# Kernel tuning notes

Measured on AMD Instinct MI355X. Metric: run time of the kernel, lower is better.

Reference implementation:

```python
import jax, jax.numpy as jnp
import numpy as np

N, M, K = 40000, 20000, 16
IN_DIM, HID, OUT_DIM, H = 64, 128, 128, 4
DH = HID // H
SIGMA_A = 15.0
FACTOR_A = 180.0 / (SIGMA_A * np.pi)  # angle (rad) -> embedding index, GeoTransformer convention
EPS = 1e-5


def sinusoidal_embed(x, d_model):
    """GeoTransformer-style sinusoidal embedding, interleaved [sin0,cos0,sin1,cos1,...]."""
    div = jnp.exp(jnp.arange(0, d_model, 2, dtype=jnp.float32) * (-np.log(10000.0) / d_model))
    omegas = x[..., None] * div  # (..., d_model/2)
    emb = jnp.stack([jnp.sin(omegas), jnp.cos(omegas)], axis=-1)
    return emb.reshape(*x.shape, d_model)


def setup_inputs() -> dict:
    key = jax.random.key(0)
    ks = jax.random.split(key, 16)

    def lin(k, i, o):
        return jax.random.normal(k, (i, o), jnp.float32) * (1.0 / np.sqrt(i))

    return {
        "feats": jax.random.normal(ks[0], (N, IN_DIM), jnp.float32),
        "node_idx": jax.random.randint(ks[1], (M,), 0, N, dtype=jnp.int32),
        "group_idx": jax.random.randint(ks[2], (M, K), 0, N, dtype=jnp.int32),
        "ppfs": jax.random.uniform(ks[3], (M, K, 4), jnp.float32, 0.0, np.pi),
        # PPF structural embedding projection
        "W_a": lin(ks[4], HID, HID), "b_a": jnp.zeros((HID,), jnp.float32),
        # input projection
        "W_in": lin(ks[5], IN_DIM, HID), "b_in": jnp.zeros((HID,), jnp.float32),
        # attention q/k/v/p projections
        "W_q": lin(ks[6], HID, HID), "b_q": jnp.zeros((HID,), jnp.float32),
        "W_k": lin(ks[7], HID, HID), "b_k": jnp.zeros((HID,), jnp.float32),
        "W_v": lin(ks[8], HID, HID), "b_v": jnp.zeros((HID,), jnp.float32),
        "W_p": lin(ks[9], HID, HID), "b_p": jnp.zeros((HID,), jnp.float32),
        # attention output linear + layernorm
        "W_o": lin(ks[10], HID, HID), "b_o": jnp.zeros((HID,), jnp.float32),
        "ln_g": jnp.ones((HID,), jnp.float32), "ln_b": jnp.zeros((HID,), jnp.float32),
        # output projection
        "W_out": lin(ks[11], HID, OUT_DIM), "b_out": jnp.zeros((OUT_DIM,), jnp.float32),
    }


def reference(feats, node_idx, group_idx, ppfs,
              W_a, b_a, W_in, b_in, W_q, b_q, W_k, b_k, W_v, b_v, W_p, b_p,
              W_o, b_o, ln_g, ln_b, W_out, b_out):
    # --- PPF structural embedding: sinusoidal per angle, linear, max over 4 angles ---
    a_emb = sinusoidal_embed(ppfs * FACTOR_A, HID)          # (M, K, 4, HID)
    a_emb = a_emb @ W_a + b_a
    pos = jnp.max(a_emb, axis=2)                            # (M, K, HID)

    # --- input projection ---
    f = feats @ W_in + b_in                                 # (N, HID)

    # --- local RPE multi-head attention ---
    q = (f @ W_q + b_q)[node_idx].reshape(M, H, DH)         # (M, H, DH)
    k = (f @ W_k + b_k)[group_idx].reshape(M, K, H, DH)     # (M, K, H, DH)
    v = (f @ W_v + b_v)[group_idx].reshape(M, K, H, DH)
    p = (pos @ W_p + b_p).reshape(M, K, H, DH)

    scores = jnp.einsum('mhd,mkhd->mhk', q, k + p) / np.sqrt(DH)  # (M, H, K)
    attn = jax.nn.softmax(scores, axis=-1)
    o = jnp.einsum('mhk,mkhd->mhd', attn, v).reshape(M, HID)

    # --- output linear + residual + layernorm ---
    hidden = o @ W_o + b_o
    res = f[node_idx] + hidden
    mu = jnp.mean(res, axis=-1, keepdims=True)
    var = jnp.var(res, axis=-1, keepdims=True)
    normed = (res - mu) * jax.lax.rsqrt(var + EPS) * ln_g + ln_b

    # --- final projection ---
    return normed @ W_out + b_out                           # (M, OUT_DIM)
```

## Files before the change

### kernel.cpp

```cpp
#include <hip/hip_runtime.h>

#define TQ 4096

__device__ __forceinline__ ushort f2bf(float x) {
  union { float f; unsigned u; } v; v.f = x;
  unsigned r = v.u + 0x7FFFu + ((v.u >> 16) & 1u);
  return (ushort)(r >> 16);
}
__device__ __forceinline__ float bf2f(ushort u) {
  union { unsigned u; float f; } v; v.u = ((unsigned)u) << 16;
  return v.f;
}

__global__ __launch_bounds__(256) void build_table(
    const float* __restrict__ W_a, const float* __restrict__ b_a,
    float* __restrict__ T) {
  __shared__ float sS[8][64], cS[8][64];
  int t = threadIdx.x;
  int row0 = blockIdx.x * 8;
  for (int i = t; i < 512; i += 256) {
    int r = i >> 6, j = i & 63;
    float x = (float)(row0 + r) * (12.0f / (float)(TQ - 1));
    float theta = expf(-(float)j * (9.210340371976184f / 64.0f));
    float om = x * theta;
    sS[r][j] = sinf(om);
    cS[r][j] = cosf(om);
  }
  __syncthreads();
  int c = t & 127, half = t >> 7;
  float b = b_a[c];
  float a0 = b, a1 = b, a2 = b, a3 = b;
  int r = half * 4;
  for (int j = 0; j < 64; ++j) {
    float ws = W_a[(2 * j) * 128 + c];
    float wc = W_a[(2 * j + 1) * 128 + c];
    a0 += sS[r + 0][j] * ws + cS[r + 0][j] * wc;
    a1 += sS[r + 1][j] * ws + cS[r + 1][j] * wc;
    a2 += sS[r + 2][j] * ws + cS[r + 2][j] * wc;
    a3 += sS[r + 3][j] * ws + cS[r + 3][j] * wc;
  }
  int rr = row0 + r;
  T[(size_t)(rr + 0) * 128 + c] = a0;
  T[(size_t)(rr + 1) * 128 + c] = a1;
  T[(size_t)(rr + 2) * 128 + c] = a2;
  T[(size_t)(rr + 3) * 128 + c] = a3;
}

__global__ __launch_bounds__(256) void weight_prep1(
    const float* __restrict__ W_in, const float* __restrict__ b_in,
    const float* __restrict__ W_q, const float* __restrict__ b_q,
    const float* __restrict__ W_k, const float* __restrict__ b_k,
    const float* __restrict__ W_v, const float* __restrict__ b_v,
    float* __restrict__ Wkv, float* __restrict__ bkv,
    float* __restrict__ Wbig, float* __restrict__ bbig) {
  __shared__ float WinS[64 * 128];
  __shared__ float binS[128];
  int t = threadIdx.x;
  for (int i = t; i < 8192; i += 256) WinS[i] = W_in[i];
  if (t < 128) binS[t] = b_in[t];
  __syncthreads();
  const float* W; const float* b;
  int which = blockIdx.x;
  if (which == 0) { W = W_q; b = b_q; }
  else if (which == 1) { W = W_k; b = b_k; }
  else { W = W_v; b = b_v; }
  int c = t & 127, ih = t >> 7;
  float acc[32] = {};
  float bacc = 0.f;
  for (int o = 0; o < 128; ++o) {
    float wv = W[o * 128 + c];
    bacc += binS[o] * wv;
#pragma unroll
    for (int j = 0; j < 32; ++j) acc[j] += WinS[(ih * 32 + j) * 128 + o] * wv;
  }
  bacc += b[c];
  if (which == 0) {
#pragma unroll
    for (int j = 0; j < 32; ++j) {
      int i = ih * 32 + j;
      Wbig[i * 768 + c] = acc[j];
      Wbig[i * 768 + 128 + c] = WinS[i * 128 + c];
    }
    if (ih == 0) { bbig[c] = bacc; bbig[128 + c] = binS[c]; }
  } else if (which == 1) {
#pragma unroll
    for (int j = 0; j < 32; ++j) Wkv[(ih * 32 + j) * 256 + c] = acc[j];
    if (ih == 0) bkv[c] = bacc;
  } else {
#pragma unroll
    for (int j = 0; j < 32; ++j) Wkv[(ih * 32 + j) * 256 + 128 + c] = acc[j];
    if (ih == 0) bkv[128 + c] = bacc;
  }
}

__global__ __launch_bounds__(256) void weight_prep2(
    const float* __restrict__ W_p, float* Wbig, float* bbig) {
  __shared__ float WcqS[64][33];
  __shared__ float bcqS[32];
  int t = threadIdx.x;
  int blk = blockIdx.x;
  int h = blk >> 1;
  for (int idx = t; idx < 2048; idx += 256) {
    int i = idx >> 5, d = idx & 31;
    WcqS[i][d] = Wbig[i * 768 + h * 32 + d];
  }
  if (t < 32) bcqS[t] = bbig[h * 32 + t];
  __syncthreads();
  int hc = blk * 64 + (t & 63);
  int c = hc & 127;
  int rg = t >> 6;
  float acc[16] = {};
  float bacc = 0.f;
  for (int d = 0; d < 32; ++d) {
    float wp = W_p[c * 128 + h * 32 + d];
    bacc += bcqS[d] * wp;
#pragma unroll
    for (int j = 0; j < 16; ++j) acc[j] += WcqS[rg * 16 + j][d] * wp;
  }
#pragma unroll
  for (int j = 0; j < 16; ++j) Wbig[(rg * 16 + j) * 768 + 256 + hc] = acc[j];
  if (rg == 0) bbig[256 + hc] = bacc;
}

__global__ __launch_bounds__(256) void proj_kv(
    const float* __restrict__ feats, const float* __restrict__ Wkv,
    const float* __restrict__ bkv, float* __restrict__ kv) {
  __shared__ float fTS[64][20];
  int t = threadIdx.x;
  int row0 = blockIdx.x * 16;
#pragma unroll
  for (int ii = 0; ii < 4; ++ii) {
    int idx = ii * 256 + t;
    int r = idx >> 6, i = idx & 63;
    fTS[i][r] = feats[(size_t)(row0 + r) * 64 + i];
  }
  __syncthreads();
  int c = t;
  float bv = bkv[c];
  float acc[16];
#pragma unroll
  for (int j = 0; j < 16; ++j) acc[j] = bv;
  for (int i = 0; i < 64; ++i) {
    float w = Wkv[i * 256 + c];
    float fv[16];
    *(float4*)&fv[0]  = *(const float4*)&fTS[i][0];
    *(float4*)&fv[4]  = *(const float4*)&fTS[i][4];
    *(float4*)&fv[8]  = *(const float4*)&fTS[i][8];
    *(float4*)&fv[12] = *(const float4*)&fTS[i][12];
#pragma unroll
    for (int j = 0; j < 16; ++j) acc[j] += fv[j] * w;
  }
#pragma unroll
  for (int j = 0; j < 16; ++j) kv[(size_t)(row0 + j) * 256 + c] = acc[j];
}

__global__ __launch_bounds__(256) void proj_m(
    const float* __restrict__ feats, const int* __restrict__ node_idx,
    const float* __restrict__ Wbig, const float* __restrict__ bbig,
    float* __restrict__ mrow) {
  __shared__ float fTS[64][12];
  int t = threadIdx.x;
  int m0 = blockIdx.x * 8;
#pragma unroll
  for (int ii = 0; ii < 2; ++ii) {
    int idx = ii * 256 + t;
    int r = idx >> 6, i = idx & 63;
    int ni = node_idx[m0 + r];
    fTS[i][r] = feats[(size_t)ni * 64 + i];
  }
  __syncthreads();
  int c = t;
  float a0[8], a1[8], a2[8];
  float b0 = bbig[c], b1 = bbig[256 + c], b2 = bbig[512 + c];
#pragma unroll
  for (int j = 0; j < 8; ++j) { a0[j] = b0; a1[j] = b1; a2[j] = b2; }
  for (int i = 0; i < 64; ++i) {
    float w0 = Wbig[i * 768 + c];
    float w1 = Wbig[i * 768 + 256 + c];
    float w2 = Wbig[i * 768 + 512 + c];
    float fv[8];
    *(float4*)&fv[0] = *(const float4*)&fTS[i][0];
    *(float4*)&fv[4] = *(const float4*)&fTS[i][4];
#pragma unroll
    for (int j = 0; j < 8; ++j) {
      a0[j] += fv[j] * w0; a1[j] += fv[j] * w1; a2[j] += fv[j] * w2;
    }
  }
#pragma unroll
  for (int j = 0; j < 8; ++j) {
    size_t base = (size_t)(m0 + j) * 768;
    mrow[base + c] = a0[j];
    mrow[base + 256 + c] = a1[j];
    mrow[base + 512 + c] = a2[j];
  }
}

__global__ __launch_bounds__(256) void attn_fused(
    const float* __restrict__ kv, const float* __restrict__ mrow,
    const float* __restrict__ T, const float* __restrict__ ppfs,
    const int* __restrict__ group_idx, float* __restrict__ o_out) {
  __shared__ ushort posW[4][16][136];
  __shared__ float qpW[4][4][132];
  __shared__ float qW[4][4][36];
  __shared__ float attnW[4][64];
  __shared__ float ppfW[4][64];
  __shared__ int gW[4][16];

  int t = threadIdx.x;
  int w = t >> 6;
  int lane = t & 63;
  int m = blockIdx.x * 4 + w;
  const float* mr = mrow + (size_t)m * 768;

  ppfW[w][lane] = ppfs[(size_t)m * 64 + lane];
  if (lane < 16) gW[w][lane] = group_idx[m * 16 + lane];
  {
    float q0 = mr[lane];
    float q1 = mr[64 + lane];
    qW[w][lane >> 5][lane & 31] = q0;
    int c1 = 64 + lane;
    qW[w][c1 >> 5][c1 & 31] = q1;
  }
#pragma unroll
  for (int i = 0; i < 8; ++i) {
    int idx = i * 64 + lane;
    qpW[w][idx >> 7][idx & 127] = mr[256 + idx];
  }
  __syncthreads();

  const float TS = (float)(TQ - 1) / 12.0f;
  int c0 = lane * 2;
#pragma unroll 4
  for (int k = 0; k < 16; ++k) {
    float p0 = -1e30f, p1 = -1e30f;
#pragma unroll
    for (int a = 0; a < 4; ++a) {
      float x = ppfW[w][k * 4 + a] * 3.8197186342054885f;
      float u = x * TS;
      int i0 = (int)u;
      i0 = min(i0, TQ - 2);
      float fr = u - (float)i0;
      const float* Tp = T + (size_t)i0 * 128 + c0;
      float2 t0 = *(const float2*)Tp;
      float2 t1 = *(const float2*)(Tp + 128);
      p0 = fmaxf(p0, t0.x + fr * (t1.x - t0.x));
      p1 = fmaxf(p1, t0.y + fr * (t1.y - t0.y));
    }
    *(ushort2*)&posW[w][k][c0] = make_ushort2(f2bf(p0), f2bf(p1));
  }
  __syncthreads();

  {
    int h = lane >> 4, k = lane & 15;
    int g = gW[w][k];
    const float* krow = kv + (size_t)g * 256 + h * 32;
    float s = 0.f;
#pragma unroll
    for (int d4 = 0; d4 < 8; ++d4) {
      float4 kvv = *(const float4*)(krow + d4 * 4);
      float4 qv = *(const float4*)&qW[w][h][d4 * 4];
      s += qv.x * kvv.x + qv.y * kvv.y + qv.z * kvv.z + qv.w * kvv.w;
    }
#pragma unroll 8
    for (int c4 = 0; c4 < 32; ++c4) {
      ushort4 pu = *(const ushort4*)&posW[w][k][c4 * 4];
      float4 qpv = *(const float4*)&qpW[w][h][c4 * 4];
      s += bf2f(pu.x) * qpv.x + bf2f(pu.y) * qpv.y +
           bf2f(pu.z) * qpv.z + bf2f(pu.w) * qpv.w;
    }
    s *= 0.17677669529663687f;
    float mx = s;
#pragma unroll
    for (int off = 1; off < 16; off <<= 1) mx = fmaxf(mx, __shfl_xor(mx, off));
    float e = __expf(s - mx);
    float sum = e;
#pragma unroll
    for (int off = 1; off < 16; off <<= 1) sum += __shfl_xor(sum, off);
    attnW[w][lane] = e / sum;
  }
  __syncthreads();

  {
    float o0 = 0.f, o1 = 0.f;
    int h0 = lane >> 4;
#pragma unroll
    for (int k = 0; k < 16; ++k) {
      float aw = attnW[w][h0 * 16 + k];
      float2 vv = *(const float2*)(kv + (size_t)gW[w][k] * 256 + 128 + c0);
      o0 += aw * vv.x;
      o1 += aw * vv.y;
    }
    *(float2*)&o_out[(size_t)m * 128 + c0] = make_float2(o0, o1);
  }
}

__global__ __launch_bounds__(256) void final_fused(
    const float* __restrict__ o, const float* __restrict__ mrow,
    const float* __restrict__ W_o, const float* __restrict__ b_o,
    const float* __restrict__ ln_g, const float* __restrict__ ln_b,
    const float* __restrict__ W_out, const float* __restrict__ b_out,
    float* __restrict__ out) {
  __shared__ float oS[16 * 128];
  __shared__ float rS[16 * 128];
  __shared__ float redS[16][2][2];
  int t = threadIdx.x;
  int m0 = blockIdx.x * 16;
  for (int i = t; i < 2048; i += 256) oS[i] = o[(size_t)m0 * 128 + i];
  __syncthreads();
  int c = t & 127, half = t >> 7;
  float acc[8];
  {
    float bv = b_o[c];
#pragma unroll
    for (int j = 0; j < 8; ++j) acc[j] = bv;
  }
  for (int i = 0; i < 128; ++i) {
    float wv = W_o[i * 128 + c];
#pragma unroll
    for (int j = 0; j < 8; ++j) acc[j] += oS[(half * 8 + j) * 128 + i] * wv;
  }
#pragma unroll
  for (int j = 0; j < 8; ++j)
    acc[j] += mrow[(size_t)(m0 + half * 8 + j) * 768 + 128 + c];
  int wih = (t >> 6) & 1;
#pragma unroll
  for (int j = 0; j < 8; ++j) {
    float s1 = acc[j], s2 = acc[j] * acc[j];
#pragma unroll
    for (int off = 1; off < 64; off <<= 1) {
      s1 += __shfl_xor(s1, off);
      s2 += __shfl_xor(s2, off);
    }
    if ((t & 63) == 0) {
      redS[half * 8 + j][wih][0] = s1;
      redS[half * 8 + j][wih][1] = s2;
    }
  }
  __syncthreads();
  float gv = ln_g[c], lb = ln_b[c];
#pragma unroll
  for (int j = 0; j < 8; ++j) {
    int row = half * 8 + j;
    float s1 = redS[row][0][0] + redS[row][1][0];
    float s2 = redS[row][0][1] + redS[row][1][1];
    float mean = s1 * (1.0f / 128.0f);
    float var = s2 * (1.0f / 128.0f) - mean * mean;
    float rstd = rsqrtf(var + 1e-5f);
    rS[row * 128 + c] = (acc[j] - mean) * rstd * gv + lb;
  }
  __syncthreads();
  float acc2[8];
  {
    float b2 = b_out[c];
#pragma unroll
    for (int j = 0; j < 8; ++j) acc2[j] = b2;
  }
  for (int i = 0; i < 128; ++i) {
    float wv = W_out[i * 128 + c];
#pragma unroll
    for (int j = 0; j < 8; ++j) acc2[j] += rS[(half * 8 + j) * 128 + i] * wv;
  }
#pragma unroll
  for (int j = 0; j < 8; ++j)
    out[(size_t)(m0 + half * 8 + j) * 128 + c] = acc2[j];
}

extern "C" void kernel_launch(void* const* d_in, const int* in_sizes, int n_in,
                              void* d_out, int out_size, void* d_ws, size_t ws_size,
                              hipStream_t stream) {
  const float* feats    = (const float*)d_in[0];
  const int*   node_idx = (const int*)d_in[1];
  const int*   group_idx= (const int*)d_in[2];
  const float* ppfs     = (const float*)d_in[3];
  const float* W_a      = (const float*)d_in[4];
  const float* b_a      = (const float*)d_in[5];
  const float* W_in     = (const float*)d_in[6];
  const float* b_in     = (const float*)d_in[7];
  const float* W_q      = (const float*)d_in[8];
  const float* b_q      = (const float*)d_in[9];
  const float* W_k      = (const float*)d_in[10];
  const float* b_k      = (const float*)d_in[11];
  const float* W_v      = (const float*)d_in[12];
  const float* b_v      = (const float*)d_in[13];
  const float* W_p      = (const float*)d_in[14];
  const float* W_o      = (const float*)d_in[16];
  const float* b_o      = (const float*)d_in[17];
  const float* ln_g     = (const float*)d_in[18];
  const float* ln_b     = (const float*)d_in[19];
  const float* W_out    = (const float*)d_in[20];
  const float* b_out    = (const float*)d_in[21];
  float* out = (float*)d_out;

  float* ws   = (float*)d_ws;
  float* kv   = ws;
  float* mrow = ws + 10240000;
  float* T    = ws + 25600000;
  float* o    = ws + 26124288;
  float* Wkv  = ws + 28684288;
  float* bkv  = ws + 28700672;
  float* Wbig = ws + 28700928;
  float* bbig = ws + 28750080;

  build_table<<<TQ / 8, 256, 0, stream>>>(W_a, b_a, T);
  weight_prep1<<<3, 256, 0, stream>>>(W_in, b_in, W_q, b_q, W_k, b_k, W_v, b_v,
                                      Wkv, bkv, Wbig, bbig);
  weight_prep2<<<8, 256, 0, stream>>>(W_p, Wbig, bbig);
  proj_kv<<<40000 / 16, 256, 0, stream>>>(feats, Wkv, bkv, kv);
  proj_m<<<20000 / 8, 256, 0, stream>>>(feats, node_idx, Wbig, bbig, mrow);
  attn_fused<<<20000 / 4, 256, 0, stream>>>(kv, mrow, T, ppfs, group_idx, o);
  final_fused<<<20000 / 16, 256, 0, stream>>>(o, mrow, W_o, b_o, ln_g, ln_b,
                                              W_out, b_out, out);
}
```

Before: 358.0 us.

## Store K/V and qp projections in bf16 and merge projection kernels

The K/V projection and the per-node qp (query times positional projection) rows are now written as bf16 instead of fp32. This halves the bytes for the random gathers in attention and for the intermediate writes. The table build, the K/V projection and the node projection are combined into one launch that branches on block index, which removes two launches and lets the independent work overlap. The cost is lower precision in K, V and qp, and register pressure set by the heaviest branch of the merged kernel.

```diff
diff --git a/kernel.cpp b/kernel.cpp
--- a/kernel.cpp
+++ b/kernel.cpp
@@ -7,43 +7,13 @@
   unsigned r = v.u + 0x7FFFu + ((v.u >> 16) & 1u);
   return (ushort)(r >> 16);
 }
-__device__ __forceinline__ float bf2f(ushort u) {
-  union { unsigned u; float f; } v; v.u = ((unsigned)u) << 16;
+__device__ __forceinline__ float bflo(unsigned u) {
+  union { unsigned u; float f; } v; v.u = u << 16;
   return v.f;
 }
-
-__global__ __launch_bounds__(256) void build_table(
-    const float* __restrict__ W_a, const float* __restrict__ b_a,
-    float* __restrict__ T) {
-  __shared__ float sS[8][64], cS[8][64];
-  int t = threadIdx.x;
-  int row0 = blockIdx.x * 8;
-  for (int i = t; i < 512; i += 256) {
-    int r = i >> 6, j = i & 63;
-    float x = (float)(row0 + r) * (12.0f / (float)(TQ - 1));
-    float theta = expf(-(float)j * (9.210340371976184f / 64.0f));
-    float om = x * theta;
-    sS[r][j] = sinf(om);
-    cS[r][j] = cosf(om);
-  }
-  __syncthreads();
-  int c = t & 127, half = t >> 7;
-  float b = b_a[c];
-  float a0 = b, a1 = b, a2 = b, a3 = b;
-  int r = half * 4;
-  for (int j = 0; j < 64; ++j) {
-    float ws = W_a[(2 * j) * 128 + c];
-    float wc = W_a[(2 * j + 1) * 128 + c];
-    a0 += sS[r + 0][j] * ws + cS[r + 0][j] * wc;
-    a1 += sS[r + 1][j] * ws + cS[r + 1][j] * wc;
-    a2 += sS[r + 2][j] * ws + cS[r + 2][j] * wc;
-    a3 += sS[r + 3][j] * ws + cS[r + 3][j] * wc;
-  }
-  int rr = row0 + r;
-  T[(size_t)(rr + 0) * 128 + c] = a0;
-  T[(size_t)(rr + 1) * 128 + c] = a1;
-  T[(size_t)(rr + 2) * 128 + c] = a2;
-  T[(size_t)(rr + 3) * 128 + c] = a3;
+__device__ __forceinline__ float bfhi(unsigned u) {
+  union { unsigned u; float f; } v; v.u = u & 0xffff0000u;
+  return v.f;
 }
 
 __global__ __launch_bounds__(256) void weight_prep1(
@@ -122,85 +92,119 @@
   if (rg == 0) bbig[256 + hc] = bacc;
 }
 
-__global__ __launch_bounds__(256) void proj_kv(
-    const float* __restrict__ feats, const float* __restrict__ Wkv,
-    const float* __restrict__ bkv, float* __restrict__ kv) {
-  __shared__ float fTS[64][20];
+__global__ __launch_bounds__(256) void mega_proj(
+    const float* __restrict__ feats, const int* __restrict__ node_idx,
+    const float* __restrict__ Wkv, const float* __restrict__ bkv,
+    const float* __restrict__ Wbig, const float* __restrict__ bbig,
+    const float* __restrict__ W_a, const float* __restrict__ b_a,
+    ushort* __restrict__ kvb, float* __restrict__ mrow,
+    ushort* __restrict__ qpb, float* __restrict__ T) {
+  __shared__ float smem[64 * 20];
   int t = threadIdx.x;
-  int row0 = blockIdx.x * 16;
-#pragma unroll
-  for (int ii = 0; ii < 4; ++ii) {
-    int idx = ii * 256 + t;
-    int r = idx >> 6, i = idx & 63;
-    fTS[i][r] = feats[(size_t)(row0 + r) * 64 + i];
-  }
-  __syncthreads();
-  int c = t;
-  float bv = bkv[c];
-  float acc[16];
-#pragma unroll
-  for (int j = 0; j < 16; ++j) acc[j] = bv;
-  for (int i = 0; i < 64; ++i) {
-    float w = Wkv[i * 256 + c];
-    float fv[16];
-    *(float4*)&fv[0]  = *(const float4*)&fTS[i][0];
-    *(float4*)&fv[4]  = *(const float4*)&fTS[i][4];
-    *(float4*)&fv[8]  = *(const float4*)&fTS[i][8];
-    *(float4*)&fv[12] = *(const float4*)&fTS[i][12];
-#pragma unroll
-    for (int j = 0; j < 16; ++j) acc[j] += fv[j] * w;
-  }
-#pragma unroll
-  for (int j = 0; j < 16; ++j) kv[(size_t)(row0 + j) * 256 + c] = acc[j];
-}
-
-__global__ __launch_bounds__(256) void proj_m(
-    const float* __restrict__ feats, const int* __restrict__ node_idx,
-    const float* __restrict__ Wbig, const float* __restrict__ bbig,
-    float* __restrict__ mrow) {
-  __shared__ float fTS[64][12];
-  int t = threadIdx.x;
-  int m0 = blockIdx.x * 8;
-#pragma unroll
-  for (int ii = 0; ii < 2; ++ii) {
-    int idx = ii * 256 + t;
-    int r = idx >> 6, i = idx & 63;
-    int ni = node_idx[m0 + r];
-    fTS[i][r] = feats[(size_t)ni * 64 + i];
-  }
-  __syncthreads();
-  int c = t;
-  float a0[8], a1[8], a2[8];
-  float b0 = bbig[c], b1 = bbig[256 + c], b2 = bbig[512 + c];
-#pragma unroll
-  for (int j = 0; j < 8; ++j) { a0[j] = b0; a1[j] = b1; a2[j] = b2; }
-  for (int i = 0; i < 64; ++i) {
-    float w0 = Wbig[i * 768 + c];
-    float w1 = Wbig[i * 768 + 256 + c];
-    float w2 = Wbig[i * 768 + 512 + c];
-    float fv[8];
-    *(float4*)&fv[0] = *(const float4*)&fTS[i][0];
-    *(float4*)&fv[4] = *(const float4*)&fTS[i][4];
+  int b = blockIdx.x;
+  if (b < 2500) {
+    float (*fTS)[20] = (float(*)[20])smem;
+    int row0 = b * 16;
+#pragma unroll
+    for (int ii = 0; ii < 4; ++ii) {
+      int idx = ii * 256 + t;
+      int r = idx >> 6, i = idx & 63;
+      fTS[i][r] = feats[(size_t)(row0 + r) * 64 + i];
+    }
+    __syncthreads();
+    int c = t;
+    float bv = bkv[c];
+    float acc[16];
+#pragma unroll
+    for (int j = 0; j < 16; ++j) acc[j] = bv;
+    for (int i = 0; i < 64; ++i) {
+      float w = Wkv[i * 256 + c];
+      float fv[16];
+      *(float4*)&fv[0]  = *(const float4*)&fTS[i][0];
+      *(float4*)&fv[4]  = *(const float4*)&fTS[i][4];
+      *(float4*)&fv[8]  = *(const float4*)&fTS[i][8];
+      *(float4*)&fv[12] = *(const float4*)&fTS[i][12];
+#pragma unroll
+      for (int j = 0; j < 16; ++j) acc[j] += fv[j] * w;
+    }
+#pragma unroll
+    for (int j = 0; j < 16; ++j)
+      kvb[(size_t)(row0 + j) * 256 + c] = f2bf(acc[j]);
+  } else if (b < 5000) {
+    float (*fTS)[12] = (float(*)[12])smem;
+    int m0 = (b - 2500) * 8;
+#pragma unroll
+    for (int ii = 0; ii < 2; ++ii) {
+      int idx = ii * 256 + t;
+      int r = idx >> 6, i = idx & 63;
+      int ni = node_idx[m0 + r];
+      fTS[i][r] = feats[(size_t)ni * 64 + i];
+    }
+    __syncthreads();
+    int c = t;
+    float a0[8], a1[8], a2[8];
+    float b0 = bbig[c], b1 = bbig[256 + c], b2 = bbig[512 + c];
+#pragma unroll
+    for (int j = 0; j < 8; ++j) { a0[j] = b0; a1[j] = b1; a2[j] = b2; }
+    for (int i = 0; i < 64; ++i) {
+      float w0 = Wbig[i * 768 + c];
+      float w1 = Wbig[i * 768 + 256 + c];
+      float w2 = Wbig[i * 768 + 512 + c];
+      float fv[8];
+      *(float4*)&fv[0] = *(const float4*)&fTS[i][0];
+      *(float4*)&fv[4] = *(const float4*)&fTS[i][4];
+#pragma unroll
+      for (int j = 0; j < 8; ++j) {
+        a0[j] += fv[j] * w0; a1[j] += fv[j] * w1; a2[j] += fv[j] * w2;
+      }
+    }
 #pragma unroll
     for (int j = 0; j < 8; ++j) {
-      a0[j] += fv[j] * w0; a1[j] += fv[j] * w1; a2[j] += fv[j] * w2;
-    }
-  }
-#pragma unroll
-  for (int j = 0; j < 8; ++j) {
-    size_t base = (size_t)(m0 + j) * 768;
-    mrow[base + c] = a0[j];
-    mrow[base + 256 + c] = a1[j];
-    mrow[base + 512 + c] = a2[j];
+      int m = m0 + j;
+      mrow[(size_t)m * 256 + c] = a0[j];
+      qpb[(size_t)m * 512 + c] = f2bf(a1[j]);
+      qpb[(size_t)m * 512 + 256 + c] = f2bf(a2[j]);
+    }
+  } else {
+    float (*sS)[64] = (float(*)[64])smem;
+    float (*cS)[64] = (float(*)[64])(smem + 512);
+    int row0 = (b - 5000) * 8;
+    for (int i = t; i < 512; i += 256) {
+      int r = i >> 6, j = i & 63;
+      float x = (float)(row0 + r) * (12.0f / (float)(TQ - 1));
+      float theta = expf(-(float)j * (9.210340371976184f / 64.0f));
+      float om = x * theta;
+      sS[r][j] = sinf(om);
+      cS[r][j] = cosf(om);
+    }
+    __syncthreads();
+    int c = t & 127, half = t >> 7;
+    float bb = b_a[c];
+    float a0 = bb, a1 = bb, a2 = bb, a3 = bb;
+    int r = half * 4;
+    for (int j = 0; j < 64; ++j) {
+      float ws = W_a[(2 * j) * 128 + c];
+      float wc = W_a[(2 * j + 1) * 128 + c];
+      a0 += sS[r + 0][j] * ws + cS[r + 0][j] * wc;
+      a1 += sS[r + 1][j] * ws + cS[r + 1][j] * wc;
+      a2 += sS[r + 2][j] * ws + cS[r + 2][j] * wc;
+      a3 += sS[r + 3][j] * ws + cS[r + 3][j] * wc;
+    }
+    int rr = row0 + r;
+    T[(size_t)(rr + 0) * 128 + c] = a0;
+    T[(size_t)(rr + 1) * 128 + c] = a1;
+    T[(size_t)(rr + 2) * 128 + c] = a2;
+    T[(size_t)(rr + 3) * 128 + c] = a3;
   }
 }
 
 __global__ __launch_bounds__(256) void attn_fused(
-    const float* __restrict__ kv, const float* __restrict__ mrow,
-    const float* __restrict__ T, const float* __restrict__ ppfs,
-    const int* __restrict__ group_idx, float* __restrict__ o_out) {
-  __shared__ ushort posW[4][16][136];
-  __shared__ float qpW[4][4][132];
+    const ushort* __restrict__ kvb, const float* __restrict__ mrow,
+    const ushort* __restrict__ qpb, const float* __restrict__ T,
+    const float* __restrict__ ppfs, const int* __restrict__ group_idx,
+    float* __restrict__ o_out) {
+  __shared__ unsigned posW[4][16][68];
+  __shared__ unsigned qpW[4][4][68];
   __shared__ float qW[4][4][36];
   __shared__ float attnW[4][64];
   __shared__ float ppfW[4][64];
@@ -210,10 +214,10 @@
   int w = t >> 6;
   int lane = t & 63;
   int m = blockIdx.x * 4 + w;
-  const float* mr = mrow + (size_t)m * 768;
 
   ppfW[w][lane] = ppfs[(size_t)m * 64 + lane];
   if (lane < 16) gW[w][lane] = group_idx[m * 16 + lane];
+  const float* mr = mrow + (size_t)m * 256;
   {
     float q0 = mr[lane];
     float q1 = mr[64 + lane];
@@ -221,10 +225,14 @@
     int c1 = 64 + lane;
     qW[w][c1 >> 5][c1 & 31] = q1;
   }
-#pragma unroll
-  for (int i = 0; i < 8; ++i) {
-    int idx = i * 64 + lane;
-    qpW[w][idx >> 7][idx & 127] = mr[256 + idx];
+  {
+    uint4 qpu = ((const uint4*)(qpb + (size_t)m * 512))[lane];
+    int j = lane * 4;
+    int h = j >> 6, j2 = j & 63;
+    qpW[w][h][j2 + 0] = qpu.x;
+    qpW[w][h][j2 + 1] = qpu.y;
+    qpW[w][h][j2 + 2] = qpu.z;
+    qpW[w][h][j2 + 3] = qpu.w;
   }
   __syncthreads();
 
@@ -246,27 +254,31 @@
       p0 = fmaxf(p0, t0.x + fr * (t1.x - t0.x));
       p1 = fmaxf(p1, t0.y + fr * (t1.y - t0.y));
     }
-    *(ushort2*)&posW[w][k][c0] = make_ushort2(f2bf(p0), f2bf(p1));
+    posW[w][k][lane] = (unsigned)f2bf(p0) | ((unsigned)f2bf(p1) << 16);
   }
   __syncthreads();
 
   {
     int h = lane >> 4, k = lane & 15;
     int g = gW[w][k];
-    const float* krow = kv + (size_t)g * 256 + h * 32;
+    const uint4* kp = (const uint4*)(kvb + (size_t)g * 256 + h * 32);
     float s = 0.f;
 #pragma unroll
-    for (int d4 = 0; d4 < 8; ++d4) {
-      float4 kvv = *(const float4*)(krow + d4 * 4);
-      float4 qv = *(const float4*)&qW[w][h][d4 * 4];
-      s += qv.x * kvv.x + qv.y * kvv.y + qv.z * kvv.z + qv.w * kvv.w;
+    for (int d8 = 0; d8 < 4; ++d8) {
+      uint4 kk = kp[d8];
+      float4 qv0 = *(const float4*)&qW[w][h][d8 * 8];
+      float4 qv1 = *(const float4*)&qW[w][h][d8 * 8 + 4];
+      s += qv0.x * bflo(kk.x) + qv0.y * bfhi(kk.x) +
+           qv0.z * bflo(kk.y) + qv0.w * bfhi(kk.y) +
+           qv1.x * bflo(kk.z) + qv1.y * bfhi(kk.z) +
+           qv1.z * bflo(kk.w) + qv1.w * bfhi(kk.w);
     }
 #pragma unroll 8
     for (int c4 = 0; c4 < 32; ++c4) {
-      ushort4 pu = *(const ushort4*)&posW[w][k][c4 * 4];
-      float4 qpv = *(const float4*)&qpW[w][h][c4 * 4];
-      s += bf2f(pu.x) * qpv.x + bf2f(pu.y) * qpv.y +
-           bf2f(pu.z) * qpv.z + bf2f(pu.w) * qpv.w;
+      unsigned pu0 = posW[w][k][2 * c4], pu1 = posW[w][k][2 * c4 + 1];
+      unsigned qu0 = qpW[w][h][2 * c4], qu1 = qpW[w][h][2 * c4 + 1];
+      s += bflo(pu0) * bflo(qu0) + bfhi(pu0) * bfhi(qu0) +
+           bflo(pu1) * bflo(qu1) + bfhi(pu1) * bfhi(qu1);
     }
     s *= 0.17677669529663687f;
     float mx = s;
@@ -286,9 +298,9 @@
 #pragma unroll
     for (int k = 0; k < 16; ++k) {
       float aw = attnW[w][h0 * 16 + k];
-      float2 vv = *(const float2*)(kv + (size_t)gW[w][k] * 256 + 128 + c0);
-      o0 += aw * vv.x;
-      o1 += aw * vv.y;
+      unsigned vv = *(const unsigned*)(kvb + (size_t)gW[w][k] * 256 + 128 + c0);
+      o0 += aw * bflo(vv);
+      o1 += aw * bfhi(vv);
     }
     *(float2*)&o_out[(size_t)m * 128 + c0] = make_float2(o0, o1);
   }
@@ -321,7 +333,7 @@
   }
 #pragma unroll
   for (int j = 0; j < 8; ++j)
-    acc[j] += mrow[(size_t)(m0 + half * 8 + j) * 768 + 128 + c];
+    acc[j] += mrow[(size_t)(m0 + half * 8 + j) * 256 + 128 + c];
   int wih = (t >> 6) & 1;
 #pragma unroll
   for (int j = 0; j < 8; ++j) {
@@ -392,22 +404,22 @@
   float* out = (float*)d_out;
 
   float* ws   = (float*)d_ws;
-  float* kv   = ws;
-  float* mrow = ws + 10240000;
-  float* T    = ws + 25600000;
-  float* o    = ws + 26124288;
-  float* Wkv  = ws + 28684288;
-  float* bkv  = ws + 28700672;
-  float* Wbig = ws + 28700928;
-  float* bbig = ws + 28750080;
-
-  build_table<<<TQ / 8, 256, 0, stream>>>(W_a, b_a, T);
+  ushort* kvb = (ushort*)ws;
+  float* mrow = ws + 5120000;
+  ushort* qpb = (ushort*)(ws + 10240000);
+  float* T    = ws + 15360000;
+  float* o    = ws + 15884288;
+  float* Wkv  = ws + 18444288;
+  float* bkv  = ws + 18460672;
+  float* Wbig = ws + 18460928;
+  float* bbig = ws + 18510080;
+
   weight_prep1<<<3, 256, 0, stream>>>(W_in, b_in, W_q, b_q, W_k, b_k, W_v, b_v,
                                       Wkv, bkv, Wbig, bbig);
   weight_prep2<<<8, 256, 0, stream>>>(W_p, Wbig, bbig);
-  proj_kv<<<40000 / 16, 256, 0, stream>>>(feats, Wkv, bkv, kv);
-  proj_m<<<20000 / 8, 256, 0, stream>>>(feats, node_idx, Wbig, bbig, mrow);
-  attn_fused<<<20000 / 4, 256, 0, stream>>>(kv, mrow, T, ppfs, group_idx, o);
+  mega_proj<<<5512, 256, 0, stream>>>(feats, node_idx, Wkv, bkv, Wbig, bbig,
+                                      W_a, b_a, kvb, mrow, qpb, T);
+  attn_fused<<<20000 / 4, 256, 0, stream>>>(kvb, mrow, qpb, T, ppfs, group_idx, o);
   final_fused<<<20000 / 16, 256, 0, stream>>>(o, mrow, W_o, b_o, ln_g, ln_b,
                                               W_out, b_out, out);
 }
```

New measurement: 331.6 us. 1.08x faster.
